# Optimization experiments

Measured on AMD Instinct MI355X. Metric: run time of the kernel, lower is better.

The kernel has to match this reference:

```python
import jax, jax.numpy as jnp
import numpy as np

T_V = 0.1
T_Q = 0.1
NEG_VIDEO_IOU = 0.5
POS_VIDEO_TOPK = 1
MARGIN = 0.0
EPS = 1e-12


def _normalize(x):
    # F.normalize(dim=-1) with eps clamp
    n = jnp.linalg.norm(x, axis=-1, keepdims=True)
    return x / jnp.maximum(n, EPS)


def _log_cross_entropy(pos_score, all_score, neg_mask, t, m):
    pos_exp = jnp.exp((pos_score - m) / t)
    neg_exp_sum = jnp.sum(jnp.exp(all_score / t) * neg_mask, axis=-1)
    loss = -((pos_score - m) / t - jnp.log(pos_exp + neg_exp_sum))
    return jnp.mean(loss)


def setup_inputs() -> dict:
    B, C, N, S = 32, 256, 64, 64
    key = jax.random.key(0)
    k1, k2, k3 = jax.random.split(key, 3)
    video_feats = jax.random.normal(k1, (B, C, N, N), dtype=jnp.float32)
    sents_feats = jax.random.normal(k2, (S, C), dtype=jnp.float32)
    iou2ds = jax.random.uniform(k3, (S, N, N), dtype=jnp.float32)
    mask2d = jnp.triu(jnp.ones((N, N), dtype=bool))  # P = N*(N+1)/2 = 2080
    num_targets = jnp.full((B,), S // B, dtype=jnp.int32)  # sums to S
    return {"video_feats": video_feats, "sents_feats": sents_feats,
            "num_targets": num_targets, "iou2ds": iou2ds, "mask2d": mask2d}


def reference(video_feats, sents_feats, num_targets, iou2ds, mask2d):
    B, C, N, _ = video_feats.shape
    S = sents_feats.shape[0]
    K = POS_VIDEO_TOPK
    # mask2d / num_targets are structural constants -> resolve on host
    flat_idx = np.nonzero(np.asarray(mask2d).reshape(-1))[0]   # [P]
    P = flat_idx.shape[0]
    scatter_idx = np.repeat(np.arange(B), np.asarray(num_targets))  # [S]

    # masked_select of valid proposals
    vf = video_feats.reshape(B, C, N * N)[:, :, flat_idx]      # [B,C,P]
    vf = jnp.transpose(vf, (0, 2, 1))                          # [B,P,C]
    iou = iou2ds.reshape(S, N * N)[:, flat_idx]                # [S,P]

    vf = _normalize(vf)
    sf = _normalize(sents_feats)                               # [S,C]

    # top-k proposals per sentence
    topk_idx = jax.lax.top_k(iou, K)[1]                        # [S,K]
    sv = vf[scatter_idx]                                       # [S,P,C]
    topk_video = jnp.take_along_axis(sv, topk_idx[:, :, None], axis=1)  # [S,K,C]

    # inter-video loss
    inter_video_pos = jnp.einsum('skc,sc->sk', topk_video, sf)          # [S,K]
    inter_video_all = jnp.einsum('skc,tc->skt', topk_video, sf)         # [S,K,S]
    inter_video_neg_mask = (~jnp.eye(S, dtype=bool))[:, None, :]        # [S,1,S]
    loss_inter_video = _log_cross_entropy(
        inter_video_pos, inter_video_all, inter_video_neg_mask, T_V, MARGIN)

    # inter-query loss
    inter_query_all = jnp.einsum('sc,bpc->sbp', sf, vf).reshape(S, 1, B * P)
    same_video = jnp.asarray(scatter_idx)[:, None] == jnp.arange(B)[None, :]  # [S,B]
    pos_mask = same_video[:, :, None] & (iou > NEG_VIDEO_IOU)[:, None, :]     # [S,B,P]
    inter_query_neg_mask = (~pos_mask).reshape(S, 1, B * P)
    loss_inter_query = _log_cross_entropy(
        inter_video_pos, inter_query_all, inter_query_neg_mask, T_Q, MARGIN)

    return (loss_inter_video, loss_inter_query)
```

## Files before the change

kernel.cpp:

```cpp
#include <hip/hip_runtime.h>
#include <hip/hip_bf16.h>
#include <math.h>

constexpr int B_ = 32;
constexpr int C_ = 256;
constexpr int N_ = 64;
constexpr int S_ = 64;
constexpr int NPIX = N_ * N_;
constexpr int P_ = 2080;
constexpr int TPB = 33;
constexpr int NQ = TPB * B_;

#define T_V_INV 10.0f
#define T_Q_INV 10.0f
#define NEG_IOU 0.5f

typedef __attribute__((ext_vector_type(8))) short short8;
typedef __attribute__((ext_vector_type(4))) float f32x4;

static __device__ __forceinline__ unsigned short f2bf(float x) {
  __hip_bfloat16 h = __float2bfloat16(x);
  unsigned short u;
  __builtin_memcpy(&u, &h, sizeof(u));
  return u;
}

__global__ __launch_bounds__(256) void k_setup(
    const float* __restrict__ sents, const float* __restrict__ iou,
    const int* __restrict__ nt,
    float* __restrict__ sf_t, unsigned short* __restrict__ sf_frag,
    int* __restrict__ scatter, int* __restrict__ top_pix,
    int* __restrict__ tab) {
  int bid = blockIdx.x, tid = threadIdx.x;
  __shared__ float wsum[4];
  __shared__ float bval[256];
  __shared__ int bidx[256];

  if (bid < S_) {
    int s = bid, c = tid;
    float v = sents[s * C_ + c];
    float ss = v * v;
    #pragma unroll
    for (int o = 32; o; o >>= 1) ss += __shfl_xor(ss, o);
    if ((c & 63) == 0) wsum[c >> 6] = ss;
    __syncthreads();
    float tot = wsum[0] + wsum[1] + wsum[2] + wsum[3];
    float rn = 1.0f / fmaxf(sqrtf(tot), 1e-12f);
    float o = v * rn;
    sf_t[c * S_ + s] = o;
    int ks = c >> 5, q = (c >> 3) & 3, j = c & 7;
    int mt = s >> 4, m = s & 15;
    sf_frag[((ks * 4 + mt) * 64 + (q * 16 + m)) * 8 + j] = f2bf(o);

    float bv = -1.0f;
    int bi = 0x7fffffff;
    for (int pix = tid; pix < NPIX; pix += 256) {
      int r = pix >> 6, c0 = pix & 63;
      if (c0 >= r) {
        float x = iou[s * NPIX + pix];
        if (x > bv) { bv = x; bi = pix; }
      }
    }
    bval[tid] = bv; bidx[tid] = bi;
    __syncthreads();
    for (int st = 128; st; st >>= 1) {
      if (tid < st) {
        float ov = bval[tid + st]; int oi = bidx[tid + st];
        if (ov > bval[tid] || (ov == bval[tid] && oi < bidx[tid])) {
          bval[tid] = ov; bidx[tid] = oi;
        }
      }
      __syncthreads();
    }
    if (tid == 0) top_pix[s] = bidx[0];
  } else {
    if (tid < S_) {
      int cum = 0, res = 0;
      for (int b = 0; b < B_; b++) {
        int nb = nt[b];
        if (tid >= cum && tid < cum + nb) res = b;
        cum += nb;
      }
      scatter[tid] = res;
    }
    for (int pix = tid; pix < NPIX; pix += 256) {
      int r = pix >> 6, c0 = pix & 63;
      if (c0 >= r) {
        int t = r * 64 - (r * (r - 1)) / 2 + (c0 - r);
        tab[t] = pix;
      }
    }
  }
}

__global__ __launch_bounds__(256) void k_main(
    const float* __restrict__ V, const float* __restrict__ iou,
    const short8* __restrict__ Afrag, const float* __restrict__ sf_t,
    const int* __restrict__ scatter, const int* __restrict__ top_pix,
    const int* __restrict__ tab,
    float* __restrict__ partials, float* __restrict__ pos_score,
    float* __restrict__ loss_vid) {
  __shared__ int ssc[S_];
  __shared__ float part[4][S_];
  __shared__ short8 afr[32 * 64];
  __shared__ float vh[C_];
  __shared__ float red[4];
  __shared__ float pdm[4][S_];

  int tid = threadIdx.x;

  if (blockIdx.x < NQ) {
    if (tid < S_) ssc[tid] = scatter[tid];
    for (int i = tid; i < 32 * 64; i += 256) afr[i] = Afrag[i];
    __syncthreads();

    int v = blockIdx.x / TPB, blk = blockIdx.x % TPB;
    int w = tid >> 6, lane = tid & 63;
    int n = lane & 15, q = lane >> 4;
    int t = blk * 64 + w * 16 + n;
    bool valid = (t < P_);
    int tt = valid ? t : (P_ - 1);
    int pix = tab[tt];

    const float* vb = V + (size_t)v * C_ * NPIX + pix;
    const float* vbq = vb + (size_t)(q * 8) * NPIX;

    float vv[64];
    #pragma unroll
    for (int ks = 0; ks < 8; ks++) {
      #pragma unroll
      for (int j = 0; j < 8; j++) {
        vv[ks * 8 + j] = vbq[(size_t)(ks * 32 + j) * NPIX];
      }
    }

    f32x4 acc[4] = {f32x4{0,0,0,0}, f32x4{0,0,0,0}, f32x4{0,0,0,0}, f32x4{0,0,0,0}};
    float ssq = 0.0f;

    #pragma unroll
    for (int ks = 0; ks < 8; ks++) {
      short8 bfrag;
      #pragma unroll
      for (int j = 0; j < 8; j++) {
        float x = vv[ks * 8 + j];
        ssq = fmaf(x, x, ssq);
        bfrag[j] = (short)f2bf(x);
      }
      #pragma unroll
      for (int mt = 0; mt < 4; mt++) {
        short8 a = afr[(ks * 4 + mt) * 64 + lane];
        acc[mt] = __builtin_amdgcn_mfma_f32_16x16x32_bf16(a, bfrag, acc[mt], 0, 0, 0);
      }
    }

    ssq += __shfl_xor(ssq, 16);
    ssq += __shfl_xor(ssq, 32);
    float rs = T_Q_INV / fmaxf(sqrtf(ssq), 1e-12f);

    #pragma unroll
    for (int mt = 0; mt < 4; mt++) {
      #pragma unroll
      for (int rr = 0; rr < 4; rr++) {
        int s = mt * 16 + q * 4 + rr;
        float e = valid ? __expf(acc[mt][rr] * rs) : 0.0f;
        if (valid && ssc[s] == v) {
          if (iou[s * NPIX + pix] > NEG_IOU) e = 0.0f;
        }
        e += __shfl_xor(e, 1);
        e += __shfl_xor(e, 2);
        e += __shfl_xor(e, 4);
        e += __shfl_xor(e, 8);
        if (n == 0) part[w][s] = e;
      }
    }
    __syncthreads();
    if (tid < S_) {
      partials[(size_t)blockIdx.x * S_ + tid] =
          part[0][tid] + part[1][tid] + part[2][tid] + part[3][tid];
    }
  } else {
    int s = blockIdx.x - NQ;
    int b = scatter[s];
    int pix = top_pix[s];
    float v = V[((size_t)b * C_ + tid) * NPIX + pix];
    float ss = v * v;
    #pragma unroll
    for (int o = 32; o; o >>= 1) ss += __shfl_xor(ss, o);
    if ((tid & 63) == 0) red[tid >> 6] = ss;
    __syncthreads();
    float tot = red[0] + red[1] + red[2] + red[3];
    float rn = 1.0f / fmaxf(sqrtf(tot), 1e-12f);
    vh[tid] = v * rn;
    __syncthreads();
    int so = tid & 63, chunk = tid >> 6;
    float pd = 0.0f;
    #pragma unroll 8
    for (int c = chunk * 64; c < chunk * 64 + 64; c++)
      pd = fmaf(vh[c], sf_t[c * S_ + so], pd);
    pdm[chunk][so] = pd;
    __syncthreads();
    if (tid < S_) {
      float dot = pdm[0][tid] + pdm[1][tid] + pdm[2][tid] + pdm[3][tid];
      if (tid == s) pos_score[s] = dot;
      float pos = __shfl(dot, s);
      float e = (tid == s) ? 0.0f : __expf(dot * T_V_INV);
      #pragma unroll
      for (int o = 32; o; o >>= 1) e += __shfl_xor(e, o);
      if (tid == 0) {
        float pp = pos * T_V_INV;
        loss_vid[s] = -(pp - logf(__expf(pp) + e));
      }
    }
  }
}

__global__ __launch_bounds__(1024) void k_fin(
    const float* __restrict__ partials, const float* __restrict__ pos_score,
    const float* __restrict__ loss_vid, float* __restrict__ out) {
  int tid = threadIdx.x;
  __shared__ f32x4 m[64][16];
  const f32x4* p4 = (const f32x4*)partials;
  int s4 = tid & 15, g = tid >> 4;
  f32x4 a = {0.0f, 0.0f, 0.0f, 0.0f};
  #pragma unroll 4
  for (int i = g; i < NQ; i += 64) a += p4[i * 16 + s4];
  m[g][s4] = a;
  __syncthreads();
  if (tid < S_) {
    int q4 = tid >> 2, e4 = tid & 3;
    float neg = 0.0f;
    #pragma unroll
    for (int g2 = 0; g2 < 64; g2++) neg += m[g2][q4][e4];
    float p = pos_score[tid] * T_Q_INV;
    float lq = -(p - logf(__expf(p) + neg));
    float lv = loss_vid[tid];
    #pragma unroll
    for (int o = 32; o; o >>= 1) {
      lq += __shfl_xor(lq, o);
      lv += __shfl_xor(lv, o);
    }
    if (tid == 0) {
      out[0] = lv / (float)S_;
      out[1] = lq / (float)S_;
    }
  }
}

extern "C" void kernel_launch(void* const* d_in, const int* in_sizes, int n_in,
                              void* d_out, int out_size, void* d_ws, size_t ws_size,
                              hipStream_t stream) {
  const float* V     = (const float*)d_in[0];
  const float* sents = (const float*)d_in[1];
  const int*   nt    = (const int*)d_in[2];
  const float* iou   = (const float*)d_in[3];

  float* ws = (float*)d_ws;
  float*          sf_t    = ws;
  unsigned short* sf_frag = (unsigned short*)(ws + 16384);
  int*   scatter   = (int*)(ws + 16384 + 8192);
  int*   top_pix   = scatter + S_;
  float* pos_score = (float*)(top_pix + S_);
  float* loss_vid  = pos_score + S_;
  int*   tab       = (int*)(loss_vid + S_);
  float* partials  = (float*)(tab + TPB * 64);

  k_setup<<<S_ + 1, 256, 0, stream>>>(sents, iou, nt, sf_t, sf_frag, scatter,
                                      top_pix, tab);
  k_main <<<NQ + S_, 256, 0, stream>>>(V, iou, (const short8*)sf_frag, sf_t,
                                       scatter, top_pix, tab, partials,
                                       pos_score, loss_vid);
  k_fin  <<<1, 1024, 0, stream>>>(partials, pos_score, loss_vid, (float*)d_out);
}
```

Before: 213.4 us.

## Fuse setup, main and finalize kernels into one launch with last-block reduction

Merges the three kernels into a single kernel. Each query block now recomputes the sentence normalization and bf16 MFMA fragments itself and derives the pixel index analytically instead of reading a table. The top-k search moves into the per-sentence blocks, and the final reduction is done by whichever block arrives last at an atomic counter. This removes two launch boundaries and the serialization between them. In exchange, all 1056 query blocks redundantly load and normalize the 64x256 sentence matrix, and a memset is added to reset the counter.

```diff
diff --git a/kernel.cpp b/kernel.cpp
--- a/kernel.cpp
+++ b/kernel.cpp
@@ -10,6 +10,7 @@
 constexpr int P_ = 2080;
 constexpr int TPB = 33;
 constexpr int NQ = TPB * B_;
+constexpr int TOTAL = NQ + S_;
 
 #define T_V_INV 10.0f
 #define T_Q_INV 10.0f
@@ -25,55 +26,38 @@
   return u;
 }
 
-__global__ __launch_bounds__(256) void k_setup(
-    const float* __restrict__ sents, const float* __restrict__ iou,
-    const int* __restrict__ nt,
-    float* __restrict__ sf_t, unsigned short* __restrict__ sf_frag,
-    int* __restrict__ scatter, int* __restrict__ top_pix,
-    int* __restrict__ tab) {
-  int bid = blockIdx.x, tid = threadIdx.x;
-  __shared__ float wsum[4];
-  __shared__ float bval[256];
-  __shared__ int bidx[256];
-
-  if (bid < S_) {
-    int s = bid, c = tid;
-    float v = sents[s * C_ + c];
-    float ss = v * v;
-    #pragma unroll
-    for (int o = 32; o; o >>= 1) ss += __shfl_xor(ss, o);
-    if ((c & 63) == 0) wsum[c >> 6] = ss;
-    __syncthreads();
-    float tot = wsum[0] + wsum[1] + wsum[2] + wsum[3];
-    float rn = 1.0f / fmaxf(sqrtf(tot), 1e-12f);
-    float o = v * rn;
-    sf_t[c * S_ + s] = o;
-    int ks = c >> 5, q = (c >> 3) & 3, j = c & 7;
-    int mt = s >> 4, m = s & 15;
-    sf_frag[((ks * 4 + mt) * 64 + (q * 16 + m)) * 8 + j] = f2bf(o);
-
-    float bv = -1.0f;
-    int bi = 0x7fffffff;
-    for (int pix = tid; pix < NPIX; pix += 256) {
-      int r = pix >> 6, c0 = pix & 63;
-      if (c0 >= r) {
-        float x = iou[s * NPIX + pix];
-        if (x > bv) { bv = x; bi = pix; }
-      }
-    }
-    bval[tid] = bv; bidx[tid] = bi;
-    __syncthreads();
-    for (int st = 128; st; st >>= 1) {
-      if (tid < st) {
-        float ov = bval[tid + st]; int oi = bidx[tid + st];
-        if (ov > bval[tid] || (ov == bval[tid] && oi < bidx[tid])) {
-          bval[tid] = ov; bidx[tid] = oi;
-        }
-      }
-      __syncthreads();
-    }
-    if (tid == 0) top_pix[s] = bidx[0];
-  } else {
+union SMem {
+  struct {
+    short8 afr[32 * 64];
+    float rns[S_];
+    int ssc[S_];
+    float scr[4][S_];
+  } q;
+  struct {
+    float vh[C_];
+    float rns[S_];
+    float scr[4][S_];
+    float red[4];
+    float bval[256];
+    int bidx[256];
+  } v;
+  struct {
+    f32x4 m[16][16];
+  } f;
+};
+
+__global__ __launch_bounds__(256) void k_all(
+    const float* __restrict__ V, const float* __restrict__ sents,
+    const int* __restrict__ nt, const float* __restrict__ iou,
+    float* __restrict__ partials, float* __restrict__ pos_score,
+    float* __restrict__ loss_vid, int* __restrict__ cnt,
+    float* __restrict__ out) {
+  __shared__ SMem sm;
+  __shared__ int s_last;
+  int tid = threadIdx.x;
+  int bx = blockIdx.x;
+
+  if (bx < NQ) {
     if (tid < S_) {
       int cum = 0, res = 0;
       for (int b = 0; b < B_; b++) {
@@ -81,48 +65,62 @@
         if (tid >= cum && tid < cum + nb) res = b;
         cum += nb;
       }
-      scatter[tid] = res;
-    }
-    for (int pix = tid; pix < NPIX; pix += 256) {
-      int r = pix >> 6, c0 = pix & 63;
-      if (c0 >= r) {
-        int t = r * 64 - (r * (r - 1)) / 2 + (c0 - r);
-        tab[t] = pix;
-      }
-    }
-  }
-}
-
-__global__ __launch_bounds__(256) void k_main(
-    const float* __restrict__ V, const float* __restrict__ iou,
-    const short8* __restrict__ Afrag, const float* __restrict__ sf_t,
-    const int* __restrict__ scatter, const int* __restrict__ top_pix,
-    const int* __restrict__ tab,
-    float* __restrict__ partials, float* __restrict__ pos_score,
-    float* __restrict__ loss_vid) {
-  __shared__ int ssc[S_];
-  __shared__ float part[4][S_];
-  __shared__ short8 afr[32 * 64];
-  __shared__ float vh[C_];
-  __shared__ float red[4];
-  __shared__ float pdm[4][S_];
-
-  int tid = threadIdx.x;
-
-  if (blockIdx.x < NQ) {
-    if (tid < S_) ssc[tid] = scatter[tid];
-    for (int i = tid; i < 32 * 64; i += 256) afr[i] = Afrag[i];
-    __syncthreads();
-
-    int v = blockIdx.x / TPB, blk = blockIdx.x % TPB;
+      sm.q.ssc[tid] = res;
+    }
+    int sa = tid & 63, chA = tid >> 6;
+    const f32x4* sp = (const f32x4*)(sents + sa * C_ + chA * 64);
+    f32x4 val[16];
+    float ssqA = 0.0f;
+    #pragma unroll
+    for (int k = 0; k < 16; k++) {
+      val[k] = sp[k];
+      ssqA += val[k][0] * val[k][0] + val[k][1] * val[k][1] +
+              val[k][2] * val[k][2] + val[k][3] * val[k][3];
+    }
+    sm.q.scr[chA][sa] = ssqA;
+    __syncthreads();
+    if (tid < S_) {
+      float tot = sm.q.scr[0][tid] + sm.q.scr[1][tid] +
+                  sm.q.scr[2][tid] + sm.q.scr[3][tid];
+      sm.q.rns[tid] = 1.0f / fmaxf(sqrtf(tot), 1e-12f);
+    }
+    __syncthreads();
+    {
+      float rn = sm.q.rns[sa];
+      int mt0 = sa >> 4, m0 = sa & 15;
+      #pragma unroll
+      for (int u = 0; u < 8; u++) {
+        int c0 = chA * 64 + u * 8;
+        int ks = c0 >> 5, qq = (c0 >> 3) & 3;
+        f32x4 a = val[u * 2], b = val[u * 2 + 1];
+        short8 e;
+        e[0] = (short)f2bf(a[0] * rn); e[1] = (short)f2bf(a[1] * rn);
+        e[2] = (short)f2bf(a[2] * rn); e[3] = (short)f2bf(a[3] * rn);
+        e[4] = (short)f2bf(b[0] * rn); e[5] = (short)f2bf(b[1] * rn);
+        e[6] = (short)f2bf(b[2] * rn); e[7] = (short)f2bf(b[3] * rn);
+        sm.q.afr[((ks * 4 + mt0) << 6) + (qq * 16 + m0)] = e;
+      }
+    }
+    __syncthreads();
+
+    int vid = bx / TPB, blk = bx % TPB;
     int w = tid >> 6, lane = tid & 63;
     int n = lane & 15, q = lane >> 4;
     int t = blk * 64 + w * 16 + n;
     bool valid = (t < P_);
     int tt = valid ? t : (P_ - 1);
-    int pix = tab[tt];
-
-    const float* vb = V + (size_t)v * C_ * NPIX + pix;
+    float disc = 16641.0f - 8.0f * (float)tt;
+    int r = (int)((129.0f - sqrtf(disc)) * 0.5f);
+    int cum = (129 * r - r * r) >> 1;
+    if (tt < cum) {
+      r -= 1; cum = (129 * r - r * r) >> 1;
+    } else {
+      int cn = (129 * (r + 1) - (r + 1) * (r + 1)) >> 1;
+      if (tt >= cn) { r += 1; cum = cn; }
+    }
+    int pix = r * 64 + (r + (tt - cum));
+
+    const float* vb = V + (size_t)vid * C_ * NPIX + pix;
     const float* vbq = vb + (size_t)(q * 8) * NPIX;
 
     float vv[64];
@@ -148,7 +146,7 @@
       }
       #pragma unroll
       for (int mt = 0; mt < 4; mt++) {
-        short8 a = afr[(ks * 4 + mt) * 64 + lane];
+        short8 a = sm.q.afr[(ks * 4 + mt) * 64 + lane];
         acc[mt] = __builtin_amdgcn_mfma_f32_16x16x32_bf16(a, bfrag, acc[mt], 0, 0, 0);
       }
     }
@@ -163,44 +161,92 @@
       for (int rr = 0; rr < 4; rr++) {
         int s = mt * 16 + q * 4 + rr;
         float e = valid ? __expf(acc[mt][rr] * rs) : 0.0f;
-        if (valid && ssc[s] == v) {
+        if (valid && sm.q.ssc[s] == vid) {
           if (iou[s * NPIX + pix] > NEG_IOU) e = 0.0f;
         }
         e += __shfl_xor(e, 1);
         e += __shfl_xor(e, 2);
         e += __shfl_xor(e, 4);
         e += __shfl_xor(e, 8);
-        if (n == 0) part[w][s] = e;
-      }
-    }
-    __syncthreads();
-    if (tid < S_) {
-      partials[(size_t)blockIdx.x * S_ + tid] =
-          part[0][tid] + part[1][tid] + part[2][tid] + part[3][tid];
+        if (n == 0) sm.q.scr[w][s] = e;
+      }
+    }
+    __syncthreads();
+    if (tid < S_) {
+      partials[(size_t)bx * S_ + tid] =
+          sm.q.scr[0][tid] + sm.q.scr[1][tid] + sm.q.scr[2][tid] + sm.q.scr[3][tid];
     }
   } else {
-    int s = blockIdx.x - NQ;
-    int b = scatter[s];
-    int pix = top_pix[s];
-    float v = V[((size_t)b * C_ + tid) * NPIX + pix];
-    float ss = v * v;
+    int s = bx - NQ;
+    int cum = 0, b = 0;
+    for (int i = 0; i < B_; i++) {
+      int nb = nt[i];
+      if (s >= cum && s < cum + nb) b = i;
+      cum += nb;
+    }
+    float bv = -1.0f;
+    int bi = 0x7fffffff;
+    for (int p0 = tid; p0 < NPIX; p0 += 256) {
+      int rr = p0 >> 6, cc = p0 & 63;
+      if (cc >= rr) {
+        float x = iou[s * NPIX + p0];
+        if (x > bv) { bv = x; bi = p0; }
+      }
+    }
+    sm.v.bval[tid] = bv; sm.v.bidx[tid] = bi;
+    __syncthreads();
+    for (int st = 128; st; st >>= 1) {
+      if (tid < st) {
+        float ov = sm.v.bval[tid + st]; int oi = sm.v.bidx[tid + st];
+        if (ov > sm.v.bval[tid] || (ov == sm.v.bval[tid] && oi < sm.v.bidx[tid])) {
+          sm.v.bval[tid] = ov; sm.v.bidx[tid] = oi;
+        }
+      }
+      __syncthreads();
+    }
+    int pix = sm.v.bidx[0];
+
+    int t = tid & 63, chA = tid >> 6;
+    const f32x4* sp = (const f32x4*)(sents + t * C_ + chA * 64);
+    f32x4 val[16];
+    float ssqA = 0.0f;
+    #pragma unroll
+    for (int k = 0; k < 16; k++) {
+      val[k] = sp[k];
+      ssqA += val[k][0] * val[k][0] + val[k][1] * val[k][1] +
+              val[k][2] * val[k][2] + val[k][3] * val[k][3];
+    }
+    sm.v.scr[chA][t] = ssqA;
+
+    float vraw = V[((size_t)b * C_ + tid) * NPIX + pix];
+    float ss = vraw * vraw;
     #pragma unroll
     for (int o = 32; o; o >>= 1) ss += __shfl_xor(ss, o);
-    if ((tid & 63) == 0) red[tid >> 6] = ss;
-    __syncthreads();
-    float tot = red[0] + red[1] + red[2] + red[3];
-    float rn = 1.0f / fmaxf(sqrtf(tot), 1e-12f);
-    vh[tid] = v * rn;
-    __syncthreads();
-    int so = tid & 63, chunk = tid >> 6;
+    if ((tid & 63) == 0) sm.v.red[tid >> 6] = ss;
+    __syncthreads();
+    if (tid < S_) {
+      float totS = sm.v.scr[0][tid] + sm.v.scr[1][tid] +
+                   sm.v.scr[2][tid] + sm.v.scr[3][tid];
+      sm.v.rns[tid] = 1.0f / fmaxf(sqrtf(totS), 1e-12f);
+    }
+    float totV = sm.v.red[0] + sm.v.red[1] + sm.v.red[2] + sm.v.red[3];
+    float rnv = 1.0f / fmaxf(sqrtf(totV), 1e-12f);
+    sm.v.vh[tid] = vraw * rnv;
+    __syncthreads();
+    float rnt = sm.v.rns[t];
     float pd = 0.0f;
-    #pragma unroll 8
-    for (int c = chunk * 64; c < chunk * 64 + 64; c++)
-      pd = fmaf(vh[c], sf_t[c * S_ + so], pd);
-    pdm[chunk][so] = pd;
-    __syncthreads();
-    if (tid < S_) {
-      float dot = pdm[0][tid] + pdm[1][tid] + pdm[2][tid] + pdm[3][tid];
+    #pragma unroll
+    for (int k = 0; k < 16; k++) {
+      int c = chA * 64 + k * 4;
+      pd += sm.v.vh[c] * val[k][0] + sm.v.vh[c + 1] * val[k][1] +
+            sm.v.vh[c + 2] * val[k][2] + sm.v.vh[c + 3] * val[k][3];
+    }
+    pd *= rnt;
+    sm.v.scr[chA][t] = pd;
+    __syncthreads();
+    if (tid < S_) {
+      float dot = sm.v.scr[0][tid] + sm.v.scr[1][tid] +
+                  sm.v.scr[2][tid] + sm.v.scr[3][tid];
       if (tid == s) pos_score[s] = dot;
       float pos = __shfl(dot, s);
       float e = (tid == s) ? 0.0f : __expf(dot * T_V_INV);
@@ -212,36 +258,36 @@
       }
     }
   }
-}
-
-__global__ __launch_bounds__(1024) void k_fin(
-    const float* __restrict__ partials, const float* __restrict__ pos_score,
-    const float* __restrict__ loss_vid, float* __restrict__ out) {
-  int tid = threadIdx.x;
-  __shared__ f32x4 m[64][16];
-  const f32x4* p4 = (const f32x4*)partials;
-  int s4 = tid & 15, g = tid >> 4;
-  f32x4 a = {0.0f, 0.0f, 0.0f, 0.0f};
-  #pragma unroll 4
-  for (int i = g; i < NQ; i += 64) a += p4[i * 16 + s4];
-  m[g][s4] = a;
+
+  __threadfence();
   __syncthreads();
-  if (tid < S_) {
-    int q4 = tid >> 2, e4 = tid & 3;
-    float neg = 0.0f;
-    #pragma unroll
-    for (int g2 = 0; g2 < 64; g2++) neg += m[g2][q4][e4];
-    float p = pos_score[tid] * T_Q_INV;
-    float lq = -(p - logf(__expf(p) + neg));
-    float lv = loss_vid[tid];
-    #pragma unroll
-    for (int o = 32; o; o >>= 1) {
-      lq += __shfl_xor(lq, o);
-      lv += __shfl_xor(lv, o);
-    }
-    if (tid == 0) {
-      out[0] = lv / (float)S_;
-      out[1] = lq / (float)S_;
+  if (tid == 0) s_last = (atomicAdd(cnt, 1) == TOTAL - 1) ? 1 : 0;
+  __syncthreads();
+  if (s_last) {
+    __threadfence();
+    const f32x4* p4 = (const f32x4*)partials;
+    int s4 = tid & 15, g = tid >> 4;
+    f32x4 a = {0.0f, 0.0f, 0.0f, 0.0f};
+    for (int k = 0; k < 66; k++)
+      a += p4[(size_t)(g + (k << 4)) * 16 + s4];
+    sm.f.m[g][s4] = a;
+    __syncthreads();
+    if (tid < S_) {
+      float neg = 0.0f;
+      #pragma unroll
+      for (int g2 = 0; g2 < 16; g2++) neg += sm.f.m[g2][tid >> 2][tid & 3];
+      float p = pos_score[tid] * T_Q_INV;
+      float lq = -(p - logf(__expf(p) + neg));
+      float lv = loss_vid[tid];
+      #pragma unroll
+      for (int o = 32; o; o >>= 1) {
+        lq += __shfl_xor(lq, o);
+        lv += __shfl_xor(lv, o);
+      }
+      if (tid == 0) {
+        out[0] = lv / (float)S_;
+        out[1] = lq / (float)S_;
+      }
     }
   }
 }
@@ -255,19 +301,12 @@
   const float* iou   = (const float*)d_in[3];
 
   float* ws = (float*)d_ws;
-  float*          sf_t    = ws;
-  unsigned short* sf_frag = (unsigned short*)(ws + 16384);
-  int*   scatter   = (int*)(ws + 16384 + 8192);
-  int*   top_pix   = scatter + S_;
-  float* pos_score = (float*)(top_pix + S_);
+  float* partials  = ws;
+  float* pos_score = ws + (size_t)NQ * S_;
   float* loss_vid  = pos_score + S_;
-  int*   tab       = (int*)(loss_vid + S_);
-  float* partials  = (float*)(tab + TPB * 64);
-
-  k_setup<<<S_ + 1, 256, 0, stream>>>(sents, iou, nt, sf_t, sf_frag, scatter,
-                                      top_pix, tab);
-  k_main <<<NQ + S_, 256, 0, stream>>>(V, iou, (const short8*)sf_frag, sf_t,
-                                       scatter, top_pix, tab, partials,
-                                       pos_score, loss_vid);
-  k_fin  <<<1, 1024, 0, stream>>>(partials, pos_score, loss_vid, (float*)d_out);
+  int*   cnt       = (int*)(loss_vid + S_);
+
+  hipMemsetAsync(cnt, 0, sizeof(int), stream);
+  k_all<<<TOTAL, 256, 0, stream>>>(V, sents, nt, iou, partials, pos_score,
+                                   loss_vid, cnt, (float*)d_out);
 }
```

Result: slower. 387.6 us (+81.6%).
